# Optimization experiments

Hardware: AMD Instinct MI355X
Metric: run time of the kernel (lower is better)

Reference implementation:

```python
import jax, jax.numpy as jnp
import numpy as np

N, C, H, W = 4, 256, 32, 32
NH = 2                      # att_nhead
HD = C // NH                # 128 per-head dim
MAX_DIS = 7
WS = 2 * MAX_DIS + 1        # 15 window side
WW = WS * WS                # 225 window positions
T = (C / NH) ** 0.5


def _gather_idx(h, w):
    # idx[wpos, m]: flat index into zero-padded (h+14, w+14) grid of the
    # neighbor at window offset wpos for query pixel m (== F.unfold semantics)
    pw = w + 2 * MAX_DIS
    dy, dx = np.meshgrid(np.arange(WS), np.arange(WS), indexing='ij')
    ys, xs = np.meshgrid(np.arange(h), np.arange(w), indexing='ij')
    idx = (dy.reshape(-1, 1) + ys.reshape(1, -1)) * pw + (dx.reshape(-1, 1) + xs.reshape(1, -1))
    return jnp.asarray(idx, dtype=jnp.int32)  # [WW, h*w]


def setup_inputs() -> dict:
    key = jax.random.key(0)
    ks = jax.random.split(key, 14)
    s = 0.02
    return {
        'q': jax.random.normal(ks[0], (N, C, H, W), jnp.float32),
        'k': jax.random.normal(ks[1], (N, C, H, W), jnp.float32),
        'v': jax.random.normal(ks[2], (N, C, H, W), jnp.float32),
        'Wq': jax.random.normal(ks[3], (C, C), jnp.float32) * s,
        'bq': jnp.zeros((C,), jnp.float32),
        'Wk': jax.random.normal(ks[4], (C, C), jnp.float32) * s,
        'bk': jnp.zeros((C,), jnp.float32),
        'Wv': jax.random.normal(ks[5], (C, C), jnp.float32) * s,
        'bv': jnp.zeros((C,), jnp.float32),
        'Wrel': jax.random.normal(ks[6], (NH, WW, HD), jnp.float32) * s,   # grouped 1x1 conv
        'brel': jnp.zeros((NH * WW,), jnp.float32),
        'V_bias': jax.random.normal(ks[7], (NH, HD, WW), jnp.float32) * s,
        'Wfc': jax.random.normal(ks[8], (C, C), jnp.float32) * s,
        'bfc': jnp.zeros((C,), jnp.float32),
    }


def _conv1x1(x, Wt, b):
    return jnp.einsum('nchw,dc->ndhw', x, Wt) + b[None, :, None, None]


def reference(q, k, v, Wq, bq, Wk, bk, Wv, bv, Wrel, brel, V_bias, Wfc, bfc):
    n, c, h, w = q.shape
    hw = h * w
    idx = _gather_idx(h, w)                                   # [WW, hw]
    pad = ((0, 0), (0, 0), (0, 0), (MAX_DIS, MAX_DIS), (MAX_DIS, MAX_DIS))

    q = _conv1x1(q, Wq, bq)
    k = _conv1x1(k, Wk, bk)
    v = _conv1x1(v, Wv, bv)

    # grouped 1x1 conv: relative position logits, [n, NH, WW, hw]
    rel = jnp.einsum('ngcxy,gwc->ngwxy', q.reshape(n, NH, HD, h, w), Wrel)
    rel = rel + brel.reshape(NH, WW)[None, :, :, None, None]
    rel = rel.reshape(n, NH, WW, hw)

    qs = (q / T).reshape(n, NH, HD, hw)

    # unfold K via zero-pad + gather: [n, NH, HD, WW, hw]
    k_pad = jnp.pad(k.reshape(n, NH, HD, h, w), pad).reshape(n, NH, HD, -1)
    k_un = k_pad[..., idx]
    qk = jnp.einsum('ngcm,ngcwm->ngwm', qs, k_un) + rel

    # boundary mask: neighbor inside the original image
    valid = jnp.pad(jnp.ones((h, w), jnp.float32), MAX_DIS).reshape(-1)[idx] > 0
    qk = jnp.where(valid[None, None], qk, jnp.float32(-1e8))
    attn = jax.nn.softmax(qk, axis=2)                         # over window positions

    agg_bias = jnp.einsum('ngwm,gcw->mngc', attn, V_bias).reshape(hw, n, c)

    # local2global scatter + dense einsum == gather of zero-padded V
    v_pad = jnp.pad(v.reshape(n, NH, HD, h, w), pad).reshape(n, NH, HD, -1)
    v_un = v_pad[..., idx]                                    # [n, NH, HD, WW, hw]
    agg_value = jnp.einsum('ngwm,ngcwm->mngc', attn, v_un).reshape(hw, n, c)

    out = (agg_value + agg_bias) @ Wfc.T + bfc                # [hw, n, c]
    return out
```

## Files before the change

kernel.cpp:

```cpp
#include <hip/hip_runtime.h>
#include <math.h>


typedef __attribute__((ext_vector_type(8))) short short8;
typedef __attribute__((ext_vector_type(4))) short short4v;
typedef __attribute__((ext_vector_type(4))) float floatx4;

__device__ __forceinline__ short f2bf(float f) {
    unsigned u = __float_as_uint(f);
    unsigned r = (u + 0x7fffu + ((u >> 16) & 1u)) >> 16;
    return (short)r;
}
__device__ __forceinline__ float bf2f(short s) {
    return __uint_as_float(((unsigned)(unsigned short)s) << 16);
}

__global__ __launch_bounds__(64)
void conv_w(const float* __restrict__ Wq, const float* __restrict__ Wk,
            const float* __restrict__ Wv, const float* __restrict__ Wfc,
            const float* __restrict__ Wrel,
            short* __restrict__ Whi, short* __restrict__ Wlo,
            short* __restrict__ Wrh, short* __restrict__ Wrl)
{
    const int lane = threadIdx.x;
    const int n16 = lane & 15, quad = lane >> 4;
    const int z = blockIdx.z;

    if (z < 4) {
        const float* W = (z == 0 ? Wq : z == 1 ? Wk : z == 2 ? Wv : Wfc);
        const int dt = blockIdx.x, kc = blockIdx.y;
        const int d = dt * 16 + n16, cb = kc * 32 + quad * 8;
        float4 w0 = *(const float4*)&W[d * 256 + cb];
        float4 w1 = *(const float4*)&W[d * 256 + cb + 4];
        float f[8] = {w0.x, w0.y, w0.z, w0.w, w1.x, w1.y, w1.z, w1.w};
        short8 h8, l8;
#pragma unroll
        for (int j = 0; j < 8; ++j) {
            short hb = f2bf(f[j]);
            h8[j] = hb;
            l8[j] = f2bf(f[j] - bf2f(hb));
        }
        long off = (long)z * 65536 + (((long)(dt * 8 + kc) * 64) + lane) * 8;
        *(short8*)(Whi + off) = h8;
        *(short8*)(Wlo + off) = l8;
    } else {
        const int g = z - 4;
        const int wt = blockIdx.x, kc = blockIdx.y;
        if (wt >= 15 || kc >= 4) return;
        const int w = wt * 16 + n16;
        const int cb = kc * 32 + quad * 8;
        float f[8] = {0.f, 0.f, 0.f, 0.f, 0.f, 0.f, 0.f, 0.f};
        if (w < 225) {
            float4 w0 = *(const float4*)&Wrel[(long)(g * 225 + w) * 128 + cb];
            float4 w1 = *(const float4*)&Wrel[(long)(g * 225 + w) * 128 + cb + 4];
            f[0] = w0.x; f[1] = w0.y; f[2] = w0.z; f[3] = w0.w;
            f[4] = w1.x; f[5] = w1.y; f[6] = w1.z; f[7] = w1.w;
        }
        short8 h8, l8;
#pragma unroll
        for (int j = 0; j < 8; ++j) {
            short hb = f2bf(f[j]);
            h8[j] = hb;
            l8[j] = f2bf(f[j] - bf2f(hb));
        }
        long off = (long)g * 30720 + (((long)(wt * 4 + kc) * 64) + lane) * 8;
        *(short8*)(Wrh + off) = h8;
        *(short8*)(Wrl + off) = l8;
    }
}

__global__ __launch_bounds__(256)
void mfma_proj(const float* __restrict__ q, const float* __restrict__ k,
               const float* __restrict__ v,
               const short* __restrict__ Whi, const short* __restrict__ Wlo,
               const float* __restrict__ bq, const float* __restrict__ bk,
               const float* __restrict__ bv,
               short* __restrict__ qhi, short* __restrict__ qlo,
               short* __restrict__ khi, short* __restrict__ klo,
               float* __restrict__ vpad)
{
    __shared__ float st[256 * 17];
    const int tid = threadIdx.x;
    const int wave = tid >> 6, lane = tid & 63;
    const int n16 = lane & 15, quad = lane >> 4;
    const int mt16 = blockIdx.x, z = blockIdx.y;
    const int sel = z >> 2, batch = z & 3;

    const float* X = (sel == 0 ? q : sel == 1 ? k : v) + ((long)batch << 18);

    {
        const float* src = X + ((long)tid << 10) + mt16 * 16;
        float4 a0 = *(const float4*)(src);
        float4 a1 = *(const float4*)(src + 4);
        float4 a2 = *(const float4*)(src + 8);
        float4 a3 = *(const float4*)(src + 12);
        float* d = &st[tid * 17];
        d[0] = a0.x; d[1] = a0.y; d[2] = a0.z; d[3] = a0.w;
        d[4] = a1.x; d[5] = a1.y; d[6] = a1.z; d[7] = a1.w;
        d[8] = a2.x; d[9] = a2.y; d[10] = a2.z; d[11] = a2.w;
        d[12] = a3.x; d[13] = a3.y; d[14] = a3.z; d[15] = a3.w;
    }

    const float* bias = (sel == 0 ? bq : sel == 1 ? bk : bv);
    float bbv[4][4];
#pragma unroll
    for (int i = 0; i < 4; ++i) {
        float4 b4 = *(const float4*)&bias[(wave * 4 + i) * 16 + quad * 4];
        bbv[i][0] = b4.x; bbv[i][1] = b4.y; bbv[i][2] = b4.z; bbv[i][3] = b4.w;
    }
    __syncthreads();

    floatx4 acc[4] = {{0.f,0.f,0.f,0.f},{0.f,0.f,0.f,0.f},
                      {0.f,0.f,0.f,0.f},{0.f,0.f,0.f,0.f}};
    const long abase = (long)sel * 65536 + (long)lane * 8;
#pragma unroll
    for (int kc = 0; kc < 8; ++kc) {
        short8 bh, bl;
        const float* col = &st[(kc * 32 + quad * 8) * 17 + n16];
#pragma unroll
        for (int j = 0; j < 8; ++j) {
            float f = col[j * 17];
            short hb = f2bf(f);
            bh[j] = hb;
            bl[j] = f2bf(f - bf2f(hb));
        }
#pragma unroll
        for (int i = 0; i < 4; ++i) {
            const int dt = wave * 4 + i;
            short8 ahi = *(const short8*)(Whi + abase + (long)(dt * 8 + kc) * 512);
            short8 alo = *(const short8*)(Wlo + abase + (long)(dt * 8 + kc) * 512);
            acc[i] = __builtin_amdgcn_mfma_f32_16x16x32_bf16(ahi, bh, acc[i], 0, 0, 0);
            acc[i] = __builtin_amdgcn_mfma_f32_16x16x32_bf16(ahi, bl, acc[i], 0, 0, 0);
            acc[i] = __builtin_amdgcn_mfma_f32_16x16x32_bf16(alo, bh, acc[i], 0, 0, 0);
        }
    }

    if (sel == 2) {
        float* Y = vpad + (long)batch * 393216;
        const int m = mt16 * 16 + n16;
        const int row = m >> 5, col = (m & 31) + 8;
#pragma unroll
        for (int i = 0; i < 4; ++i) {
            const int dt = wave * 4 + i;
#pragma unroll
            for (int r = 0; r < 4; ++r)
                Y[(long)(dt * 16 + quad * 4 + r) * 1536 + row * 48 + col] = acc[i][r] + bbv[i][r];
        }
        {
            const int prow = mt16 >> 1, side = mt16 & 1;
            long po = (long)tid * 1536 + prow * 48 + side * 40;
            float4 zz = {0.f, 0.f, 0.f, 0.f};
            *(float4*)&Y[po] = zz;
            *(float4*)&Y[po + 4] = zz;
        }
        return;
    }

    __syncthreads();
    float* tile = st;
#pragma unroll
    for (int i = 0; i < 4; ++i) {
        const int dt = wave * 4 + i;
#pragma unroll
        for (int r = 0; r < 4; ++r)
            tile[n16 * 257 + dt * 16 + quad * 4 + r] = acc[i][r] + bbv[i][r];
    }
    __syncthreads();

    const float scale = (sel == 1) ? 0.08838834764831845f : 1.0f;
    const int m_l = tid >> 4, c16 = (tid & 15) * 16;
    const int m = mt16 * 16 + m_l;
    short* oh = sel ? khi : qhi;
    short* ol = sel ? klo : qlo;
#pragma unroll
    for (int half = 0; half < 2; ++half) {
        const int cg = c16 + half * 8;
        short8 h8, l8;
#pragma unroll
        for (int j = 0; j < 8; ++j) {
            float f = tile[m_l * 257 + cg + j] * scale;
            short hb = f2bf(f);
            h8[j] = hb;
            l8[j] = f2bf(f - bf2f(hb));
        }
        const int g = cg >> 7, ch = cg & 127;
        const long base = (((long)(batch * 2 + g) << 10) + m) * 128 + ch;
        *(short8*)(oh + base) = h8;
        *(short8*)(ol + base) = l8;
    }
}

__global__ __launch_bounds__(256)
void scores_pv(const short* __restrict__ qhi, const short* __restrict__ qlo,
               const short* __restrict__ khi, const short* __restrict__ klo,
               const short* __restrict__ Wrh, const short* __restrict__ Wrl,
               const float* __restrict__ brel,
               const float* __restrict__ vpad, const float* __restrict__ Vbias,
               short* __restrict__ AGhi, short* __restrict__ AGlo)
{
    __shared__ __align__(16) float smem[16 * 241 + 225 * 16];
    __shared__ float invl[16];
    float* qk   = smem;
    float* pa2  = smem + 16 * 241;
    float* tile = smem;

    const int tid = threadIdx.x;
    const int wave = tid >> 6, lane = tid & 63;
    const int lin = blockIdx.x;
    const int bz  = lin & 7;
    const int r2  = lin >> 3;
    const int chh = r2 & 1;
    const int yy  = r2 >> 1;
    const int y   = yy >> 1;
    const int xt  = yy & 1;
    const int g = bz & 1;
    const int x0 = xt * 16;

    const int n16 = lane & 15, quad = lane >> 4;
    const long qbase = (((long)bz << 10) + y * 32 + x0 + n16) * 128 + quad * 8;
    short8 a_hi[4], a_lo[4];
#pragma unroll
    for (int ch = 0; ch < 4; ++ch) {
        a_hi[ch] = *(const short8*)(qhi + qbase + ch * 32);
        a_lo[ch] = *(const short8*)(qlo + qbase + ch * 32);
    }

    for (int wt = wave; wt < 15; wt += 4) {
        const short* Ah = Wrh + (long)g * 30720 + ((long)(wt * 4) * 64 + lane) * 8;
        const short* Al = Wrl + (long)g * 30720 + ((long)(wt * 4) * 64 + lane) * 8;
        floatx4 racc = {0.f, 0.f, 0.f, 0.f};
#pragma unroll
        for (int kc = 0; kc < 4; ++kc) {
            short8 whh = *(const short8*)(Ah + kc * 512);
            short8 wll = *(const short8*)(Al + kc * 512);
            racc = __builtin_amdgcn_mfma_f32_16x16x32_bf16(whh, a_hi[kc], racc, 0, 0, 0);
            racc = __builtin_amdgcn_mfma_f32_16x16x32_bf16(whh, a_lo[kc], racc, 0, 0, 0);
            racc = __builtin_amdgcn_mfma_f32_16x16x32_bf16(wll, a_hi[kc], racc, 0, 0, 0);
        }
#pragma unroll
        for (int r = 0; r < 4; ++r) {
            int w = wt * 16 + quad * 4 + r;
            if (w < 225) {
                int dy = w / 15, dx = w - dy * 15;
                qk[n16 * 241 + dy * 16 + dx] = racc[r] + brel[g * 225 + w];
            }
        }
    }
    __syncthreads();

    for (int e = tid; e < 16 * 241; e += 256) {
        int px = e / 241, idx = e - px * 241;
        int dy = idx >> 4, dx = idx & 15;
        int hy = y + dy - 7, hx = x0 + px + dx - 7;
        bool valid = (dx < 15) && (dy < 15) &&
                     (hy >= 0) && (hy < 32) && (hx >= 0) && (hx < 32);
        if (!valid) qk[e] = -1e8f;
    }
    __syncthreads();

    for (int dy = wave; dy < 15; dy += 4) {
        const int ky = y + dy - 7;
        if (ky < 0 || ky > 31) continue;
#pragma unroll
        for (int kxt = 0; kxt < 2; ++kxt) {
            const int kxg = x0 - 8 + kxt * 16 + n16;
            const long kb = (((long)bz << 10) + ky * 32 + kxg) * 128 + quad * 8;
            floatx4 acc = {0.f, 0.f, 0.f, 0.f};
#pragma unroll
            for (int ch = 0; ch < 4; ++ch) {
                short8 b_hi = *(const short8*)(khi + kb + ch * 32);
                short8 b_lo = *(const short8*)(klo + kb + ch * 32);
                acc = __builtin_amdgcn_mfma_f32_16x16x32_bf16(a_hi[ch], b_hi, acc, 0, 0, 0);
                acc = __builtin_amdgcn_mfma_f32_16x16x32_bf16(a_hi[ch], b_lo, acc, 0, 0, 0);
                acc = __builtin_amdgcn_mfma_f32_16x16x32_bf16(a_lo[ch], b_hi, acc, 0, 0, 0);
            }
            if (kxg >= 0 && kxg < 32) {
#pragma unroll
                for (int r = 0; r < 4; ++r) {
                    int m = quad * 4 + r;
                    int dx = kxg - (x0 + m) + 7;
                    if (dx >= 0 && dx < 15) {
                        int s = m * 241 + dy * 16 + dx;
                        qk[s] = qk[s] + acc[r];
                    }
                }
            }
        }
    }
    __syncthreads();

    {
        int px = tid >> 4, s = tid & 15;
        float mx = -3.0e38f;
        for (int w = s; w < 240; w += 16) mx = fmaxf(mx, qk[px * 241 + w]);
#pragma unroll
        for (int msk = 8; msk; msk >>= 1) mx = fmaxf(mx, __shfl_xor(mx, msk));
        float sum = 0.f;
        for (int w = s; w < 240; w += 16) {
            float p = __expf(qk[px * 241 + w] - mx);
            qk[px * 241 + w] = p;
            sum += p;
        }
#pragma unroll
        for (int msk = 8; msk; msk >>= 1) sum += __shfl_xor(sum, msk);
        if (s == 0) invl[px] = 1.0f / sum;
    }
    __syncthreads();

    for (int e = tid; e < 3600; e += 256) {
        int w = e >> 4, px = e & 15;
        int dy2 = w / 15, dx2 = w - dy2 * 15;
        pa2[w * 16 + px] = qk[px * 241 + dy2 * 16 + dx2] * invl[px];
    }
    __syncthreads();

    const int n = bz >> 1;
    const int chg = tid >> 2;
    const int xq  = tid & 3;
    const int c0  = chh * 64 + chg;
    const int xb  = x0 + xq * 4;
    const float* v0 = vpad + (long)bz * 196608 + (long)c0 * 1536;
    const float* b0 = Vbias + (g * 128 + c0) * 225;

    float acc0[4] = {0.f, 0.f, 0.f, 0.f};

    for (int dy = 0; dy < 15; ++dy) {
        int hy = y + dy - 7;
        if (hy < 0 || hy > 31) continue;
        const float4* r0 = (const float4*)(v0 + hy * 48 + xb);
        float wa[20];
#pragma unroll
        for (int t = 0; t < 5; ++t) {
            float4 a = r0[t];
            wa[4*t+0] = a.x; wa[4*t+1] = a.y; wa[4*t+2] = a.z; wa[4*t+3] = a.w;
        }
        const float* par = &pa2[dy * 15 * 16 + xq * 4];
        const float* vb0 = b0 + dy * 15;
#pragma unroll
        for (int dx = 0; dx < 15; ++dx) {
            float4 p4 = *(const float4*)&par[dx * 16];
            float ba = vb0[dx];
            acc0[0] += p4.x * (wa[1 + dx] + ba);
            acc0[1] += p4.y * (wa[2 + dx] + ba);
            acc0[2] += p4.z * (wa[3 + dx] + ba);
            acc0[3] += p4.w * (wa[4 + dx] + ba);
        }
    }

#pragma unroll
    for (int i = 0; i < 4; ++i)
        tile[(xq * 4 + i) * 68 + chg] = acc0[i];
    __syncthreads();

    const int sub = tid >> 6;
    if (sub < 2) {
        short8 h8, l8;
#pragma unroll
        for (int j = 0; j < 8; ++j) {
            float f = tile[n16 * 68 + sub * 32 + quad * 8 + j];
            short hb = f2bf(f);
            h8[j] = hb;
            l8[j] = f2bf(f - bf2f(hb));
        }
        const int mt16 = y * 2 + xt;
        const int kc = g * 4 + chh * 2 + sub;
        long off = (long)n * 262144 + (((long)(mt16 * 8 + kc) * 64) + lane) * 8;
        *(short8*)(AGhi + off) = h8;
        *(short8*)(AGlo + off) = l8;
    }
}

__global__ __launch_bounds__(256)
void mfma_fc(const short* __restrict__ Ahi, const short* __restrict__ Alo,
             const short* __restrict__ Whi, const short* __restrict__ Wlo,
             const float* __restrict__ bfc, float* __restrict__ out)
{
    __shared__ float tile[16 * 132];
    const int tid = threadIdx.x;
    const int wave = tid >> 6, lane = tid & 63;
    const int n16 = lane & 15, quad = lane >> 4;
    const int mt16 = blockIdx.x, db2 = blockIdx.y, nz = blockIdx.z;
    const int dt0 = db2 * 8 + wave * 2;

    const short* Bh = Ahi + (long)nz * 262144;
    const short* Bl = Alo + (long)nz * 262144;
    const long abase = (long)3 * 65536 + (long)lane * 8;

    float bbv[2][4];
#pragma unroll
    for (int p = 0; p < 2; ++p) {
        float4 b4 = *(const float4*)&bfc[(dt0 + p) * 16 + quad * 4];
        bbv[p][0] = b4.x; bbv[p][1] = b4.y; bbv[p][2] = b4.z; bbv[p][3] = b4.w;
    }

    floatx4 acc[2] = {{0.f,0.f,0.f,0.f},{0.f,0.f,0.f,0.f}};
#pragma unroll
    for (int kc = 0; kc < 8; ++kc) {
        const long bo = (long)(mt16 * 8 + kc) * 512 + (long)lane * 8;
        short8 bh = *(const short8*)(Bh + bo);
        short8 bl = *(const short8*)(Bl + bo);
#pragma unroll
        for (int p = 0; p < 2; ++p) {
            const int dt = dt0 + p;
            short8 ahi = *(const short8*)(Whi + abase + (long)(dt * 8 + kc) * 512);
            short8 alo = *(const short8*)(Wlo + abase + (long)(dt * 8 + kc) * 512);
            acc[p] = __builtin_amdgcn_mfma_f32_16x16x32_bf16(ahi, bh, acc[p], 0, 0, 0);
            acc[p] = __builtin_amdgcn_mfma_f32_16x16x32_bf16(ahi, bl, acc[p], 0, 0, 0);
            acc[p] = __builtin_amdgcn_mfma_f32_16x16x32_bf16(alo, bh, acc[p], 0, 0, 0);
        }
    }

#pragma unroll
    for (int p = 0; p < 2; ++p) {
        const int dl = (wave * 2 + p) * 16 + quad * 4;
#pragma unroll
        for (int r = 0; r < 4; ++r)
            tile[n16 * 132 + dl + r] = acc[p][r] + bbv[p][r];
    }
    __syncthreads();

    const int m_l = tid >> 4, d8 = (tid & 15) * 8;
    float4 o0 = *(const float4*)&tile[m_l * 132 + d8];
    float4 o1 = *(const float4*)&tile[m_l * 132 + d8 + 4];
    long ob = (long)(mt16 * 16 + m_l) * 1024 + nz * 256 + db2 * 128 + d8;
    *(float4*)&out[ob] = o0;
    *(float4*)&out[ob + 4] = o1;
}

extern "C" void kernel_launch(void* const* d_in, const int* in_sizes, int n_in,
                              void* d_out, int out_size, void* d_ws, size_t ws_size,
                              hipStream_t stream)
{
    const float* q    = (const float*)d_in[0];
    const float* k    = (const float*)d_in[1];
    const float* v    = (const float*)d_in[2];
    const float* Wq   = (const float*)d_in[3];
    const float* bq   = (const float*)d_in[4];
    const float* Wk   = (const float*)d_in[5];
    const float* bk   = (const float*)d_in[6];
    const float* Wv   = (const float*)d_in[7];
    const float* bv   = (const float*)d_in[8];
    const float* Wrel = (const float*)d_in[9];
    const float* brel = (const float*)d_in[10];
    const float* Vb   = (const float*)d_in[11];
    const float* Wfc  = (const float*)d_in[12];
    const float* bfc  = (const float*)d_in[13];
    float* out = (float*)d_out;

    float* ws   = (float*)d_ws;
    float* vpad = ws + 2097152;
    short* qhi  = (short*)(ws + 6561792);
    short* qlo  = (short*)(ws + 7086080);
    short* khi  = (short*)(ws + 7610368);
    short* klo  = (short*)(ws + 8134656);
    short* Whi  = (short*)(ws + 11804672);
    short* Wlo  = (short*)(ws + 11935744);
    short* AGhi = (short*)(ws + 12066816);
    short* AGlo = (short*)(ws + 12591104);
    short* Wrh  = (short*)(ws + 13115392);
    short* Wrl  = (short*)(ws + 13146112);

    conv_w<<<dim3(16, 8, 6), dim3(64), 0, stream>>>(Wq, Wk, Wv, Wfc, Wrel,
                                                    Whi, Wlo, Wrh, Wrl);

    mfma_proj<<<dim3(64, 12), dim3(256), 0, stream>>>(q, k, v, Whi, Wlo,
                                                      bq, bk, bv,
                                                      qhi, qlo, khi, klo, vpad);

    scores_pv<<<dim3(1024), dim3(256), 0, stream>>>(qhi, qlo, khi, klo,
                                                    Wrh, Wrl, brel,
                                                    vpad, Vb, AGhi, AGlo);

    mfma_fc<<<dim3(64, 2, 4), dim3(256), 0, stream>>>(AGhi, AGlo, Whi, Wlo,
                                                      bfc, out);
}
```

Baseline: 171.5 us.

## Move attention-weighted V and V_bias aggregation onto split-bf16 MFMA

Replaces the scalar FP32 loop that combined attention probabilities with padded V and V_bias with bf16 hi/lo split MFMA products. V is now stored as hi/lo bf16 in a padded layout, V_bias is pre-split in conv_w, and each dy row is fed to the MFMA as a banded probability matrix built from LDS. Each block now covers all 128 channels of a head instead of 64, which halves the grid from 1024 to 512 blocks. The split-bf16 scheme keeps accuracy close to fp32, but it adds band-building work, 3x MFMA redundancy, and scattered short stores in the projection.

```diff
diff --git a/kernel.cpp b/kernel.cpp
--- a/kernel.cpp
+++ b/kernel.cpp
@@ -18,9 +18,10 @@
 __global__ __launch_bounds__(64)
 void conv_w(const float* __restrict__ Wq, const float* __restrict__ Wk,
             const float* __restrict__ Wv, const float* __restrict__ Wfc,
-            const float* __restrict__ Wrel,
+            const float* __restrict__ Wrel, const float* __restrict__ Vb,
             short* __restrict__ Whi, short* __restrict__ Wlo,
-            short* __restrict__ Wrh, short* __restrict__ Wrl)
+            short* __restrict__ Wrh, short* __restrict__ Wrl,
+            short* __restrict__ Vbh, short* __restrict__ Vbl)
 {
     const int lane = threadIdx.x;
     const int n16 = lane & 15, quad = lane >> 4;
@@ -43,7 +44,7 @@
         long off = (long)z * 65536 + (((long)(dt * 8 + kc) * 64) + lane) * 8;
         *(short8*)(Whi + off) = h8;
         *(short8*)(Wlo + off) = l8;
-    } else {
+    } else if (z < 6) {
         const int g = z - 4;
         const int wt = blockIdx.x, kc = blockIdx.y;
         if (wt >= 15 || kc >= 4) return;
@@ -66,6 +67,28 @@
         long off = (long)g * 30720 + (((long)(wt * 4 + kc) * 64) + lane) * 8;
         *(short8*)(Wrh + off) = h8;
         *(short8*)(Wrl + off) = l8;
+    } else {
+        const int g = z - 6;
+        const int dt = blockIdx.x, wk = blockIdx.y;
+        if (dt >= 8) return;
+        const int ch = dt * 16 + n16;
+        const int w0 = wk * 32 + quad * 8;
+        float f[8];
+#pragma unroll
+        for (int j = 0; j < 8; ++j) {
+            int w = w0 + j;
+            f[j] = (w < 225) ? Vb[(long)(g * 128 + ch) * 225 + w] : 0.f;
+        }
+        short8 h8, l8;
+#pragma unroll
+        for (int j = 0; j < 8; ++j) {
+            short hb = f2bf(f[j]);
+            h8[j] = hb;
+            l8[j] = f2bf(f[j] - bf2f(hb));
+        }
+        long off = (((long)(g * 128 + ch)) << 8) + w0;
+        *(short8*)(Vbh + off) = h8;
+        *(short8*)(Vbl + off) = l8;
     }
 }
 
@@ -77,7 +100,7 @@
                const float* __restrict__ bv,
                short* __restrict__ qhi, short* __restrict__ qlo,
                short* __restrict__ khi, short* __restrict__ klo,
-               float* __restrict__ vpad)
+               short* __restrict__ vhi, short* __restrict__ vlo)
 {
     __shared__ float st[256 * 17];
     const int tid = threadIdx.x;
@@ -136,22 +159,30 @@
     }
 
     if (sel == 2) {
-        float* Y = vpad + (long)batch * 393216;
         const int m = mt16 * 16 + n16;
-        const int row = m >> 5, col = (m & 31) + 8;
+        const int yq = m >> 5, col = (m & 31) + 8;
 #pragma unroll
         for (int i = 0; i < 4; ++i) {
             const int dt = wave * 4 + i;
 #pragma unroll
-            for (int r = 0; r < 4; ++r)
-                Y[(long)(dt * 16 + quad * 4 + r) * 1536 + row * 48 + col] = acc[i][r] + bbv[i][r];
+            for (int r = 0; r < 4; ++r) {
+                const int ch = dt * 16 + quad * 4 + r;
+                const int gg = ch >> 7, chh = ch & 127;
+                float f = acc[i][r] + bbv[i][r];
+                short hb = f2bf(f);
+                short lb = f2bf(f - bf2f(hb));
+                long o = (((long)((batch * 2 + gg) * 128 + chh) * 32 + yq)) * 48 + col;
+                vhi[o] = hb;
+                vlo[o] = lb;
+            }
         }
         {
             const int prow = mt16 >> 1, side = mt16 & 1;
-            long po = (long)tid * 1536 + prow * 48 + side * 40;
-            float4 zz = {0.f, 0.f, 0.f, 0.f};
-            *(float4*)&Y[po] = zz;
-            *(float4*)&Y[po + 4] = zz;
+            const int gg = tid >> 7, chp = tid & 127;
+            long po = (((long)((batch * 2 + gg) * 128 + chp) * 32 + prow)) * 48 + side * 40;
+            short8 zz = {0,0,0,0,0,0,0,0};
+            *(short8*)(vhi + po) = zz;
+            *(short8*)(vlo + po) = zz;
         }
         return;
     }
@@ -195,22 +226,20 @@
                const short* __restrict__ khi, const short* __restrict__ klo,
                const short* __restrict__ Wrh, const short* __restrict__ Wrl,
                const float* __restrict__ brel,
-               const float* __restrict__ vpad, const float* __restrict__ Vbias,
+               const short* __restrict__ vhi, const short* __restrict__ vlo,
+               const short* __restrict__ Vbh, const short* __restrict__ Vbl,
                short* __restrict__ AGhi, short* __restrict__ AGlo)
 {
-    __shared__ __align__(16) float smem[16 * 241 + 225 * 16];
+    __shared__ __align__(16) float qk[16 * 241];
+    __shared__ __align__(16) short pah[16 * 264];
+    __shared__ __align__(16) short pal[16 * 264];
     __shared__ float invl[16];
-    float* qk   = smem;
-    float* pa2  = smem + 16 * 241;
-    float* tile = smem;
 
     const int tid = threadIdx.x;
     const int wave = tid >> 6, lane = tid & 63;
     const int lin = blockIdx.x;
     const int bz  = lin & 7;
-    const int r2  = lin >> 3;
-    const int chh = r2 & 1;
-    const int yy  = r2 >> 1;
+    const int yy  = lin >> 3;
     const int y   = yy >> 1;
     const int xt  = yy & 1;
     const int g = bz & 1;
@@ -307,67 +336,96 @@
     }
     __syncthreads();
 
-    for (int e = tid; e < 3600; e += 256) {
-        int w = e >> 4, px = e & 15;
-        int dy2 = w / 15, dx2 = w - dy2 * 15;
-        pa2[w * 16 + px] = qk[px * 241 + dy2 * 16 + dx2] * invl[px];
-    }
-    __syncthreads();
-
+    for (int e = tid; e < 4096; e += 256) {
+        int px = e >> 8, w = e & 255;
+        float p = 0.f;
+        if (w < 225) {
+            int dy2 = w / 15, dx2 = w - dy2 * 15;
+            p = qk[px * 241 + dy2 * 16 + dx2] * invl[px];
+        }
+        short hb = f2bf(p);
+        pah[px * 264 + w] = hb;
+        pal[px * 264 + w] = f2bf(p - bf2f(hb));
+    }
+    __syncthreads();
+
+    floatx4 acc[2] = {{0.f,0.f,0.f,0.f},{0.f,0.f,0.f,0.f}};
+    const int ch0a = (wave * 2) * 16;
+    const int ch0b = (wave * 2 + 1) * 16;
+
+#pragma unroll
+    for (int wk = 0; wk < 8; ++wk) {
+        short8 pa_h = *(const short8*)&pah[n16 * 264 + wk * 32 + quad * 8];
+        short8 pa_l = *(const short8*)&pal[n16 * 264 + wk * 32 + quad * 8];
+        const long vb0 = (((long)(g * 128 + ch0a + n16)) << 8) + wk * 32 + quad * 8;
+        const long vb1 = (((long)(g * 128 + ch0b + n16)) << 8) + wk * 32 + quad * 8;
+        short8 b0h = *(const short8*)(Vbh + vb0);
+        short8 b0l = *(const short8*)(Vbl + vb0);
+        short8 b1h = *(const short8*)(Vbh + vb1);
+        short8 b1l = *(const short8*)(Vbl + vb1);
+        acc[0] = __builtin_amdgcn_mfma_f32_16x16x32_bf16(pa_h, b0h, acc[0], 0, 0, 0);
+        acc[0] = __builtin_amdgcn_mfma_f32_16x16x32_bf16(pa_h, b0l, acc[0], 0, 0, 0);
+        acc[0] = __builtin_amdgcn_mfma_f32_16x16x32_bf16(pa_l, b0h, acc[0], 0, 0, 0);
+        acc[1] = __builtin_amdgcn_mfma_f32_16x16x32_bf16(pa_h, b1h, acc[1], 0, 0, 0);
+        acc[1] = __builtin_amdgcn_mfma_f32_16x16x32_bf16(pa_h, b1l, acc[1], 0, 0, 0);
+        acc[1] = __builtin_amdgcn_mfma_f32_16x16x32_bf16(pa_l, b1h, acc[1], 0, 0, 0);
+    }
+
+    for (int dy = 0; dy < 15; ++dy) {
+        const int ky = y + dy - 7;
+        if (ky < 0 || ky > 31) continue;
+        short8 bnd_h, bnd_l;
+        const int rowoff = n16 * 264 + dy * 15 - n16 - 1;
+#pragma unroll
+        for (int j = 0; j < 8; ++j) {
+            int kk = quad * 8 + j;
+            int dx = kk - n16 - 1;
+            bool valid = (unsigned)dx < 15u;
+            int idx = valid ? (rowoff + kk) : 0;
+            short vh = pah[idx];
+            short vl = pal[idx];
+            bnd_h[j] = valid ? vh : (short)0;
+            bnd_l[j] = valid ? vl : (short)0;
+        }
+        const long v0o = (((long)((bz * 128 + ch0a + n16)) * 32 + ky)) * 48 + x0 + quad * 8;
+        const long v1o = (((long)((bz * 128 + ch0b + n16)) * 32 + ky)) * 48 + x0 + quad * 8;
+        short8 v0h = *(const short8*)(vhi + v0o);
+        short8 v0l = *(const short8*)(vlo + v0o);
+        short8 v1h = *(const short8*)(vhi + v1o);
+        short8 v1l = *(const short8*)(vlo + v1o);
+        acc[0] = __builtin_amdgcn_mfma_f32_16x16x32_bf16(bnd_h, v0h, acc[0], 0, 0, 0);
+        acc[0] = __builtin_amdgcn_mfma_f32_16x16x32_bf16(bnd_h, v0l, acc[0], 0, 0, 0);
+        acc[0] = __builtin_amdgcn_mfma_f32_16x16x32_bf16(bnd_l, v0h, acc[0], 0, 0, 0);
+        acc[1] = __builtin_amdgcn_mfma_f32_16x16x32_bf16(bnd_h, v1h, acc[1], 0, 0, 0);
+        acc[1] = __builtin_amdgcn_mfma_f32_16x16x32_bf16(bnd_h, v1l, acc[1], 0, 0, 0);
+        acc[1] = __builtin_amdgcn_mfma_f32_16x16x32_bf16(bnd_l, v1h, acc[1], 0, 0, 0);
+    }
+
+    float* tile = qk;
+#pragma unroll
+    for (int t = 0; t < 2; ++t) {
+        const int cb = (wave * 2 + t) * 16 + n16;
+#pragma unroll
+        for (int r = 0; r < 4; ++r)
+            tile[(quad * 4 + r) * 133 + cb] = acc[t][r];
+    }
+    __syncthreads();
+
+    const int sub = tid >> 6;
+    short8 h8, l8;
+#pragma unroll
+    for (int j = 0; j < 8; ++j) {
+        float f = tile[n16 * 133 + sub * 32 + quad * 8 + j];
+        short hb = f2bf(f);
+        h8[j] = hb;
+        l8[j] = f2bf(f - bf2f(hb));
+    }
     const int n = bz >> 1;
-    const int chg = tid >> 2;
-    const int xq  = tid & 3;
-    const int c0  = chh * 64 + chg;
-    const int xb  = x0 + xq * 4;
-    const float* v0 = vpad + (long)bz * 196608 + (long)c0 * 1536;
-    const float* b0 = Vbias + (g * 128 + c0) * 225;
-
-    float acc0[4] = {0.f, 0.f, 0.f, 0.f};
-
-    for (int dy = 0; dy < 15; ++dy) {
-        int hy = y + dy - 7;
-        if (hy < 0 || hy > 31) continue;
-        const float4* r0 = (const float4*)(v0 + hy * 48 + xb);
-        float wa[20];
-#pragma unroll
-        for (int t = 0; t < 5; ++t) {
-            float4 a = r0[t];
-            wa[4*t+0] = a.x; wa[4*t+1] = a.y; wa[4*t+2] = a.z; wa[4*t+3] = a.w;
-        }
-        const float* par = &pa2[dy * 15 * 16 + xq * 4];
-        const float* vb0 = b0 + dy * 15;
-#pragma unroll
-        for (int dx = 0; dx < 15; ++dx) {
-            float4 p4 = *(const float4*)&par[dx * 16];
-            float ba = vb0[dx];
-            acc0[0] += p4.x * (wa[1 + dx] + ba);
-            acc0[1] += p4.y * (wa[2 + dx] + ba);
-            acc0[2] += p4.z * (wa[3 + dx] + ba);
-            acc0[3] += p4.w * (wa[4 + dx] + ba);
-        }
-    }
-
-#pragma unroll
-    for (int i = 0; i < 4; ++i)
-        tile[(xq * 4 + i) * 68 + chg] = acc0[i];
-    __syncthreads();
-
-    const int sub = tid >> 6;
-    if (sub < 2) {
-        short8 h8, l8;
-#pragma unroll
-        for (int j = 0; j < 8; ++j) {
-            float f = tile[n16 * 68 + sub * 32 + quad * 8 + j];
-            short hb = f2bf(f);
-            h8[j] = hb;
-            l8[j] = f2bf(f - bf2f(hb));
-        }
-        const int mt16 = y * 2 + xt;
-        const int kc = g * 4 + chh * 2 + sub;
-        long off = (long)n * 262144 + (((long)(mt16 * 8 + kc) * 64) + lane) * 8;
-        *(short8*)(AGhi + off) = h8;
-        *(short8*)(AGlo + off) = l8;
-    }
+    const int mt16 = y * 2 + xt;
+    const int kc = g * 4 + sub;
+    long off = (long)n * 262144 + (((long)(mt16 * 8 + kc) * 64) + lane) * 8;
+    *(short8*)(AGhi + off) = h8;
+    *(short8*)(AGlo + off) = l8;
 }
 
 __global__ __launch_bounds__(256)
@@ -448,7 +506,10 @@
     float* out = (float*)d_out;
 
     float* ws   = (float*)d_ws;
-    float* vpad = ws + 2097152;
+    short* vhi  = (short*)(ws + 2097152);
+    short* vlo  = (short*)(ws + 2883584);
+    short* Vbh  = (short*)(ws + 4718592);
+    short* Vbl  = (short*)(ws + 4751360);
     short* qhi  = (short*)(ws + 6561792);
     short* qlo  = (short*)(ws + 7086080);
     short* khi  = (short*)(ws + 7610368);
@@ -460,16 +521,18 @@
     short* Wrh  = (short*)(ws + 13115392);
     short* Wrl  = (short*)(ws + 13146112);
 
-    conv_w<<<dim3(16, 8, 6), dim3(64), 0, stream>>>(Wq, Wk, Wv, Wfc, Wrel,
-                                                    Whi, Wlo, Wrh, Wrl);
+    conv_w<<<dim3(16, 8, 8), dim3(64), 0, stream>>>(Wq, Wk, Wv, Wfc, Wrel, Vb,
+                                                    Whi, Wlo, Wrh, Wrl, Vbh, Vbl);
 
     mfma_proj<<<dim3(64, 12), dim3(256), 0, stream>>>(q, k, v, Whi, Wlo,
                                                       bq, bk, bv,
-                                                      qhi, qlo, khi, klo, vpad);
-
-    scores_pv<<<dim3(1024), dim3(256), 0, stream>>>(qhi, qlo, khi, klo,
-                                                    Wrh, Wrl, brel,
-                                                    vpad, Vb, AGhi, AGlo);
+                                                      qhi, qlo, khi, klo,
+                                                      vhi, vlo);
+
+    scores_pv<<<dim3(512), dim3(256), 0, stream>>>(qhi, qlo, khi, klo,
+                                                   Wrh, Wrl, brel,
+                                                   vhi, vlo, Vbh, Vbl,
+                                                   AGhi, AGlo);
 
     mfma_fc<<<dim3(64, 2, 4), dim3(256), 0, stream>>>(AGhi, AGlo, Whi, Wlo,
                                                       bfc, out);
```

Result: faster. 162.4 us (-5.3%).
